# Kernel tuning notes

Hardware: AMD Instinct MI355X
Metric: run time of the kernel (lower is better)

## Reference

```python
import jax, jax.numpy as jnp
import numpy as np

HEAD_COUNT = 16
HEAD_DIM = 128  # embed_count // head_count = 2048 // 16


def setup_inputs() -> dict:
    key = jax.random.key(0)
    k0, k1, k2, k3, k4 = jax.random.split(key, 5)
    B, C, S = 4, 2048, 1024
    keys = jax.random.normal(k0, (B, C, 1, S), dtype=jnp.float32)
    values = jax.random.normal(k1, (B, C, 1, S), dtype=jnp.float32)
    queries = jax.random.normal(k2, (B, C, 1, S), dtype=jnp.float32)
    attention_mask = jax.random.randint(k3, (B, S), 0, 2).astype(bool)
    # guarantee at least one valid key per batch row so softmax is finite
    attention_mask = attention_mask.at[:, 0].set(True)
    w_out = jax.random.normal(k4, (C, C), dtype=jnp.float32) * 0.02
    return {"keys": keys, "values": values, "queries": queries,
            "attention_mask": attention_mask, "w_out": w_out}


def reference(keys, values, queries, attention_mask, w_out):
    B, C, _, S = keys.shape
    h, d = HEAD_COUNT, HEAD_DIM
    # keys: [B,C,1,S] -> transpose(1,3) -> [B,S,1,C] -> [B,S,h,d]
    k = jnp.transpose(keys[:, :, 0, :], (0, 2, 1)).reshape(B, S, h, d)      # bkhd
    # values/queries: [B,C,1,S] -> [B,h,d,S] -> transpose(1,2) -> [B,d,h,S]
    v = jnp.transpose(values[:, :, 0, :].reshape(B, h, d, S), (0, 2, 1, 3))  # bdhk
    q = jnp.transpose(queries[:, :, 0, :].reshape(B, h, d, S), (0, 2, 1, 3)) # bdhq
    # additive mask bias: 0 where attended, -inf where masked; broadcast over h,q
    bias = jnp.where(attention_mask, 0.0, -jnp.inf).astype(keys.dtype)       # [B,K]
    scale = 1.0 / np.sqrt(d).astype(np.float32)
    w = jnp.einsum('bdhq,bkhd->bkhq', q * scale, k)                          # [B,K,h,Q]
    w = w + bias[:, :, None, None]
    w = jax.nn.softmax(w, axis=1)  # softmax over keys (dim 1)
    hid = jnp.einsum('bkhq,bdhk->bdhq', w, v)                                # [B,d,h,Q]
    hid = jnp.transpose(hid, (0, 2, 1, 3)).reshape(B, C, S)                  # [B,C,Q]
    out = jnp.einsum('oc,bcq->boq', w_out, hid)                              # 1x1 conv out_proj
    return out.reshape(B, C, 1, S)
```

## Files before the change

### kernel.cpp

```cpp
#include <hip/hip_runtime.h>

#define Bq 4
#define Cc 2048
#define Ss 1024
#define Hh 16
#define Dd 128

#define QSCALE 0.127517429f

typedef __bf16 bf16x8 __attribute__((ext_vector_type(8)));
typedef float  f32x4  __attribute__((ext_vector_type(4)));

__device__ __forceinline__ ushort f2bf(float f) {
    uint u = __float_as_uint(f);
    u += 0x7FFFu + ((u >> 16) & 1u);
    return (ushort)(u >> 16);
}
__device__ __forceinline__ uint pack2bf(float a, float b) {
    return (uint)f2bf(a) | ((uint)f2bf(b) << 16);
}
__device__ __forceinline__ void gld16(const void* g, void* l) {
    __builtin_amdgcn_global_load_lds(
        (const __attribute__((address_space(1))) unsigned int*)g,
        (__attribute__((address_space(3))) unsigned int*)l, 16, 0, 0);
}

__global__ __launch_bounds__(256) void prep_all3(const float* __restrict__ w,
                                                 const float* __restrict__ v,
                                                 const float* __restrict__ keys,
                                                 const unsigned* __restrict__ mask,
                                                 ushort* __restrict__ wb,
                                                 ushort* __restrict__ vb,
                                                 ushort* __restrict__ Kt,
                                                 float* __restrict__ bias) {
    __shared__ __align__(16) float T[128][65];
    const int t = threadIdx.x;
    const int blk = blockIdx.x;

    if (blk < 2048) {
        const size_t e = ((size_t)blk * 256 + t) * 8;
        const int row = (int)(e >> 11), col = (int)(e & 2047);
        const int colS = (col & ~63) | ((col & 63) ^ ((row & 7) << 3));
        float4 v0 = *(const float4*)&w[e];
        float4 v1 = *(const float4*)&w[e + 4];
        uint4 o;
        o.x = pack2bf(v0.x, v0.y); o.y = pack2bf(v0.z, v0.w);
        o.z = pack2bf(v1.x, v1.y); o.w = pack2bf(v1.z, v1.w);
        *(uint4*)&wb[(size_t)row * 2048 + colS] = o;
    } else if (blk < 6144) {
        const int tid = (blk - 2048) * 256 + t;
        const int row = tid >> 7;
        const int cp = tid & 127;
        const int blk64 = (cp >> 3) * 64;
        const int j0 = cp & 7;
        const int b5 = j0 >> 2, h = j0 & 3;
        const float* src = v + (size_t)row * 1024 + blk64 + 32 * b5 + 4 * h;
        float4 A = *(const float4*)src;
        float4 B = *(const float4*)(src + 16);
        uint4 o;
        o.x = pack2bf(A.x, A.y); o.y = pack2bf(A.z, A.w);
        o.z = pack2bf(B.x, B.y); o.w = pack2bf(B.z, B.w);
        *(uint4*)&vb[(size_t)row * 1024 + blk64 + ((j0 * 8) ^ ((row & 7) << 3))] = o;
    } else if (blk < 7168) {
        const int b2 = blk - 6144;
        const int s0 = (b2 & 15) * 64;
        const int bh = b2 >> 4;
        const float* src = keys + (size_t)bh * 128 * 1024;
#pragma unroll
        for (int p = 0; p < 8; ++p) {
            const int d = p * 16 + (t >> 4);
            float4 v4 = *(const float4*)&src[(size_t)d * 1024 + s0 + (t & 15) * 4];
            T[d][(t & 15) * 4 + 0] = v4.x;
            T[d][(t & 15) * 4 + 1] = v4.y;
            T[d][(t & 15) * 4 + 2] = v4.z;
            T[d][(t & 15) * 4 + 3] = v4.w;
        }
        __syncthreads();
#pragma unroll
        for (int p = 0; p < 4; ++p) {
            const int k = p * 16 + (t >> 4);
            const int x = t & 15;
            uint4 o;
            o.x = pack2bf(T[x * 8 + 0][k], T[x * 8 + 1][k]);
            o.y = pack2bf(T[x * 8 + 2][k], T[x * 8 + 3][k]);
            o.z = pack2bf(T[x * 8 + 4][k], T[x * 8 + 5][k]);
            o.w = pack2bf(T[x * 8 + 6][k], T[x * 8 + 7][k]);
            const size_t rowbyte = ((size_t)bh * 1024 + s0 + k) * 256;
            const int boff = (x * 16) ^ ((k & 7) << 4);
            *(uint4*)((char*)Kt + rowbyte + boff) = o;
        }
    } else {
        __shared__ int f01, ff;
        if (t == 0) { f01 = 0; ff = 0; }
        __syncthreads();
        int a = 0, c = 0;
        for (int i = t; i < 1024; i += 256) {
            unsigned vv = mask[i];
            if (vv != 0u && vv != 1u) a = 1;
            if (vv != 0u && vv != 0x3F800000u) c = 1;
        }
        if (a) atomicOr(&f01, 1);
        if (c) atomicOr(&ff, 1);
        __syncthreads();
        const int mode = f01 ? (ff ? 1 : 2) : 0;
        const int* mi = (const int*)mask;
        const unsigned char* mb = (const unsigned char*)mask;
        const float* mf = (const float*)mask;
        for (int i = t; i < Bq * Ss; i += 256) {
            bool on;
            if (mode == 0)      on = (mi[i] != 0);
            else if (mode == 1) on = (mb[i] != 0);
            else                on = (mf[i] != 0.0f);
            bias[i] = on ? 0.0f : -1e30f;
        }
    }
}

__global__ __launch_bounds__(512) void attn11(const float* __restrict__ queries,
                                              const ushort* __restrict__ Kt,
                                              const ushort* __restrict__ Vbf,
                                              const float* __restrict__ bias,
                                              ushort* __restrict__ hidT) {
    __shared__ __align__(16) char SMEM[102400];
    float* biasS = (float*)(SMEM + 98304);

    const int t = threadIdx.x, l = t & 63, w = t >> 6;
    const int kk = l & 15, g = l >> 4;

    const int bid = blockIdx.x;
    const int vid = (bid & 7) * 32 + (bid >> 3);
    const int bh = vid >> 2, qt = vid & 3;
    const int b = bh >> 4, hh = bh & 15;
    const int q0 = qt * 256;
    const size_t bhbase = (size_t)bh * 1024;

    for (int i = t; i < Ss; i += 512) biasS[i] = bias[b * Ss + i];

    bf16x8 qf[2][4];
    {
        const float* Qg = queries + (size_t)(b * Cc + hh * Dd) * Ss;
        float* Qstg = (float*)SMEM;
#pragma unroll
        for (int half = 0; half < 2; ++half) {
#pragma unroll
            for (int it = 0; it < 8; ++it) {
                const int row = it * 8 + w;
                gld16(Qg + (size_t)(half * 64 + row) * 1024 + q0 + l * 4,
                      (char*)Qstg + row * 1024);
            }
            asm volatile("s_waitcnt vmcnt(0)" ::: "memory");
            __builtin_amdgcn_s_barrier();
#pragma unroll
            for (int dch = 0; dch < 2; ++dch) {
                const int dc = half * 2 + dch;
#pragma unroll
                for (int qs = 0; qs < 2; ++qs) {
                    const int q = w * 32 + qs * 16 + kk;
                    float f[8];
#pragma unroll
                    for (int j = 0; j < 8; ++j) {
                        const int dl = dc * 32 + g * 8 + j - half * 64;
                        f[j] = Qstg[dl * 256 + q];
                    }
                    uint4 u;
                    u.x = pack2bf(f[0] * QSCALE, f[1] * QSCALE);
                    u.y = pack2bf(f[2] * QSCALE, f[3] * QSCALE);
                    u.z = pack2bf(f[4] * QSCALE, f[5] * QSCALE);
                    u.w = pack2bf(f[6] * QSCALE, f[7] * QSCALE);
                    qf[qs][dc] = *(bf16x8*)&u;
                }
            }
            __builtin_amdgcn_s_barrier();
        }
    }

    float lrun[2] = {0.0f, 0.0f};
    f32x4 hacc[2][8];
#pragma unroll
    for (int qs = 0; qs < 2; ++qs)
#pragma unroll
        for (int i = 0; i < 8; ++i) hacc[qs][i] = (f32x4){0.f, 0.f, 0.f, 0.f};

#define ATTN_STAGE(bufi, cki)                                                   \
    {                                                                           \
        const int k0n = (cki) * 64;                                             \
        ushort* Kd = (ushort*)SMEM + (bufi) * 8192;                             \
        ushort* Vd = (ushort*)(SMEM + 49152) + (bufi) * 8192;                   \
        _Pragma("unroll")                                                       \
        for (int ii = 0; ii < 4; ++ii) {                                        \
            const int inst = ii * 8 + w;                                        \
            if (inst < 16) {                                                    \
                gld16(Kt + (bhbase + k0n + inst * 4 + (l >> 4)) * 128 +         \
                          (l & 15) * 8,                                         \
                      Kd + inst * 512);                                         \
            } else {                                                            \
                const int i2 = inst - 16;                                       \
                gld16(Vbf + ((size_t)bh * 128 + i2 * 8 + (l >> 3)) * 1024 +     \
                          k0n + (l & 7) * 8,                                    \
                      Vd + i2 * 512);                                           \
            }                                                                   \
        }                                                                       \
    }

#define QK_HALF(h)                                                               \
    _Pragma("unroll")                                                            \
    for (int n2 = 0; n2 < 2; ++n2) {                                             \
        const int ns = 2 * (h) + n2;                                             \
        const f32x4 ci = *(const f32x4*)&biasS[k0 + ns * 16 + g * 4];            \
        bf16x8 kf[4];                                                            \
        const ushort* kr = KTb + (ns * 16 + kk) * 128;                           \
        _Pragma("unroll")                                                        \
        for (int dc = 0; dc < 4; ++dc)                                           \
            kf[dc] = *(const bf16x8*)(kr + ((dc * 32 + g * 8) ^ ((kk & 7) << 3)));\
        _Pragma("unroll")                                                        \
        for (int qs = 0; qs < 2; ++qs) {                                         \
            f32x4 a = ci;                                                        \
            _Pragma("unroll")                                                    \
            for (int dc = 0; dc < 4; ++dc)                                       \
                a = __builtin_amdgcn_mfma_f32_16x16x32_bf16(                     \
                    kf[dc], qf[qs][dc], a, 0, 0, 0);                             \
            sc[qs][ns] = a;                                                      \
        }                                                                        \
    }

#define SM_HALF(h)                                                               \
    _Pragma("unroll")                                                            \
    for (int qs = 0; qs < 2; ++qs) {                                             \
        float pv0[4], pv1[4];                                                    \
        _Pragma("unroll")                                                        \
        for (int r = 0; r < 4; ++r) {                                            \
            pv0[r] = exp2f(sc[qs][2 * (h)][r]);                                  \
            pv1[r] = exp2f(sc[qs][2 * (h) + 1][r]);                              \
        }                                                                        \
        lrun[qs] += (pv0[0] + pv0[1] + pv0[2] + pv0[3])                          \
                  + (pv1[0] + pv1[1] + pv1[2] + pv1[3]);                         \
        bf16x8 vpk;                                                              \
        _Pragma("unroll")                                                        \
        for (int j = 0; j < 4; ++j) { vpk[j] = (__bf16)pv0[j];                   \
                                      vpk[j + 4] = (__bf16)pv1[j]; }             \
        pb[qs][h] = vpk;                                                         \
    }

#define PV_HALF(h)                                                               \
    _Pragma("unroll")                                                            \
    for (int ds = 0; ds < 8; ++ds) {                                             \
        bf16x8 vf = *(const bf16x8*)(Vsb + (ds * 16 + kk) * 64 +                 \
                        (((h) * 32 + g * 8) ^ ((kk & 7) << 3)));                 \
        hacc[0][ds] = __builtin_amdgcn_mfma_f32_16x16x32_bf16(                   \
            vf, pb[0][h], hacc[0][ds], 0, 0, 0);                                 \
        hacc[1][ds] = __builtin_amdgcn_mfma_f32_16x16x32_bf16(                   \
            vf, pb[1][h], hacc[1][ds], 0, 0, 0);                                 \
    }

#define ATTN_COMPUTE(bi, ck)                                                     \
    {                                                                            \
        const int k0 = (ck) * 64;                                                \
        const ushort* KTb = (const ushort*)SMEM + (bi) * 8192;                   \
        const ushort* Vsb = (const ushort*)(SMEM + 49152) + (bi) * 8192;         \
        f32x4 sc[2][4];                                                          \
        bf16x8 pb[2][2];                                                         \
        QK_HALF(0);                                                              \
        QK_HALF(1);                                                              \
        SM_HALF(0);                                                              \
        PV_HALF(0);                                                              \
        SM_HALF(1);                                                              \
        PV_HALF(1);                                                              \
    }

    ATTN_STAGE(0, 0);
    ATTN_STAGE(1, 1);
    asm volatile("s_waitcnt vmcnt(4)" ::: "memory");
    __builtin_amdgcn_s_barrier();

    int cb = 0, sb = 2;
    for (int ck = 0; ck < 14; ++ck) {
        ATTN_STAGE(sb, ck + 2);
        ATTN_COMPUTE(cb, ck);
        asm volatile("s_waitcnt vmcnt(4)" ::: "memory");
        __builtin_amdgcn_s_barrier();
        cb = (cb == 2) ? 0 : cb + 1;
        sb = (sb == 2) ? 0 : sb + 1;
    }
    ATTN_COMPUTE(cb, 14);
    asm volatile("s_waitcnt vmcnt(0)" ::: "memory");
    __builtin_amdgcn_s_barrier();
    cb = (cb == 2) ? 0 : cb + 1;
    ATTN_COMPUTE(cb, 15);
#undef ATTN_STAGE
#undef ATTN_COMPUTE
#undef QK_HALF
#undef SM_HALF
#undef PV_HALF

    float linv[2];
#pragma unroll
    for (int qs = 0; qs < 2; ++qs) {
        float s = lrun[qs];
        s += __shfl_xor(s, 16);
        s += __shfl_xor(s, 32);
        linv[qs] = 1.0f / s;
    }

    __syncthreads();
    {
        ushort* hs = (ushort*)SMEM;
#pragma unroll
        for (int qs = 0; qs < 2; ++qs) {
            const int row = w * 32 + qs * 16 + kk;
#pragma unroll
            for (int ds = 0; ds < 8; ++ds) {
                uint2 pk;
                pk.x = pack2bf(hacc[qs][ds][0] * linv[qs], hacc[qs][ds][1] * linv[qs]);
                pk.y = pack2bf(hacc[qs][ds][2] * linv[qs], hacc[qs][ds][3] * linv[qs]);
                const int off = row * 256 + ((ds * 32 + g * 8) ^ ((row & 7) << 4));
                *(uint2*)((char*)hs + off) = pk;
            }
        }
    }
    __syncthreads();

    const char* hsb = (const char*)SMEM;
#pragma unroll
    for (int it = 0; it < 8; ++it) {
        const int idx = it * 512 + t;
        const int q = idx >> 4, x = idx & 15;
        uint4 vv = *(const uint4*)(hsb + q * 256 + x * 16);
        *(uint4*)((char*)hidT + ((size_t)(b * Ss + q0 + q)) * 4096 + hh * 256 + x * 16) = vv;
    }
}

__global__ __launch_bounds__(512, 2) void proj5(const ushort* __restrict__ Wbf,
                                                const ushort* __restrict__ hidT,
                                                float* __restrict__ out) {
    __shared__ __align__(16) char SMEM[147456];
    const int t = threadIdx.x, l = t & 63, w = t >> 6;
    const int kk = l & 15, g = l >> 4;
    const int wr = w >> 2, wc = w & 3;

    const int bid = blockIdx.x;
    const int vid = (bid & 7) * 32 + (bid >> 3);
    const int o0 = (vid & 15) * 128;
    const int n0 = (vid >> 4) * 256;

    f32x4 acc[4][4];
#pragma unroll
    for (int i = 0; i < 4; ++i)
#pragma unroll
        for (int j = 0; j < 4; ++j) acc[i][j] = (f32x4){0.f, 0.f, 0.f, 0.f};

    const int swz = (kk & 7) << 3;

#define P5_STAGE_A(st, ks)                                                      \
    {                                                                           \
        ushort* Ad = (ushort*)SMEM + (st) * 8192;                               \
        _Pragma("unroll")                                                       \
        for (int ii = 0; ii < 2; ++ii) {                                        \
            const int idx = ii * 512 + t;                                       \
            gld16(Wbf + (size_t)(o0 + (idx >> 3)) * 2048 + (ks) * 64 +          \
                      (idx & 7) * 8,                                            \
                  Ad + idx * 8);                                                \
        }                                                                       \
    }
#define P5_STAGE_B(st, ks, p)                                                   \
    {                                                                           \
        ushort* Bd = (ushort*)(SMEM + 49152) + (st) * 16384;                    \
        _Pragma("unroll")                                                       \
        for (int jj = (p) * 2; jj < (p) * 2 + 2; ++jj) {                        \
            const int idx = jj * 512 + t;                                       \
            gld16(hidT + (size_t)(n0 + (idx >> 3)) * 2048 + (ks) * 64 +         \
                      (idx & 7) * 8,                                            \
                  Bd + idx * 8);                                                \
        }                                                                       \
    }
#define P5_READ(dcv)                                                            \
    _Pragma("unroll")                                                           \
    for (int ms = 0; ms < 4; ++ms)                                              \
        af[ms] = *(const bf16x8*)&Ab[(wr * 64 + ms * 16 + kk) * 64 +            \
                                     (((dcv) * 32 + g * 8) ^ swz)];             \
    _Pragma("unroll")                                                           \
    for (int ns = 0; ns < 4; ++ns)                                              \
        bfr[ns] = *(const bf16x8*)&Bb[(wc * 64 + ns * 16 + kk) * 64 +           \
                                      (((dcv) * 32 + g * 8) ^ swz)];
#define P5_MFMA()                                                               \
    __builtin_amdgcn_s_setprio(1);                                              \
    _Pragma("unroll")                                                           \
    for (int ms = 0; ms < 4; ++ms)                                              \
        _Pragma("unroll")                                                       \
        for (int ns = 0; ns < 4; ++ns)                                          \
            acc[ms][ns] = __builtin_amdgcn_mfma_f32_16x16x32_bf16(              \
                af[ms], bfr[ns], acc[ms][ns], 0, 0, 0);                         \
    __builtin_amdgcn_s_setprio(0);

    P5_STAGE_A(0, 0); P5_STAGE_B(0, 0, 0); P5_STAGE_B(0, 0, 1);
    P5_STAGE_A(1, 1); P5_STAGE_B(1, 1, 0); P5_STAGE_B(1, 1, 1);
    asm volatile("s_waitcnt vmcnt(6)" ::: "memory");
    __builtin_amdgcn_s_barrier();

    int ct = 0, st2 = 2;
    for (int tt = 0; tt < 32; ++tt) {
        const ushort* Ab = (const ushort*)SMEM + ct * 8192;
        const ushort* Bb = (const ushort*)(SMEM + 49152) + ct * 16384;
        bf16x8 af[4], bfr[4];

        P5_READ(0);
        if (tt < 30) { P5_STAGE_A(st2, tt + 2); P5_STAGE_B(st2, tt + 2, 0); }
        __builtin_amdgcn_s_barrier();
        asm volatile("s_waitcnt lgkmcnt(0)" ::: "memory");
        P5_MFMA();
        __builtin_amdgcn_s_barrier();

        P5_READ(1);
        if (tt < 30) P5_STAGE_B(st2, tt + 2, 1);
        if (tt < 30) { asm volatile("s_waitcnt vmcnt(6)" ::: "memory"); }
        else         { asm volatile("s_waitcnt vmcnt(0)" ::: "memory"); }
        __builtin_amdgcn_s_barrier();
        asm volatile("s_waitcnt lgkmcnt(0)" ::: "memory");
        P5_MFMA();
        __builtin_amdgcn_s_barrier();

        ct = (ct == 2) ? 0 : ct + 1;
        st2 = (st2 == 2) ? 0 : st2 + 1;
    }
#undef P5_STAGE_A
#undef P5_STAGE_B
#undef P5_READ
#undef P5_MFMA

#pragma unroll
    for (int ms = 0; ms < 4; ++ms)
#pragma unroll
        for (int ns = 0; ns < 4; ++ns) {
            const int o = o0 + wr * 64 + ms * 16 + g * 4;
            const int n = n0 + wc * 64 + ns * 16 + kk;
            const int bb = n >> 10, qq = n & 1023;
            float* op = out + ((size_t)(bb * Cc + o)) * Ss + qq;
#pragma unroll
            for (int r = 0; r < 4; ++r) op[(size_t)r * Ss] = acc[ms][ns][r];
        }
}

extern "C" void kernel_launch(void* const* d_in, const int* in_sizes, int n_in,
                              void* d_out, int out_size, void* d_ws, size_t ws_size,
                              hipStream_t stream) {
    const float*    keys    = (const float*)d_in[0];
    const float*    values  = (const float*)d_in[1];
    const float*    queries = (const float*)d_in[2];
    const unsigned* mask    = (const unsigned*)d_in[3];
    const float*    w_out   = (const float*)d_in[4];
    float* out = (float*)d_out;

    char* ws = (char*)d_ws;
    float*  bias = (float*)ws;
    ushort* Wbf  = (ushort*)(ws + 16384);
    ushort* Kt   = (ushort*)(ws + 16384 + (8u << 20));
    ushort* Vbf  = (ushort*)(ws + 16384 + (24u << 20));
    ushort* hidT = (ushort*)(ws + 16384 + (40u << 20));

    hipLaunchKernelGGL(prep_all3, dim3(7169), dim3(256), 0, stream,
                       w_out, values, keys, mask, Wbf, Vbf, Kt, bias);
    hipLaunchKernelGGL(attn11, dim3(256), dim3(512), 0, stream,
                       queries, Kt, Vbf, bias, hidT);
    hipLaunchKernelGGL(proj5, dim3(256), dim3(512), 0, stream,
                       Wbf, hidT, out);
}
```

Measured before the change: 115.8 us.

## Read K/V fragments directly from global memory in attention, drop LDS pipelining

The attention kernel no longer stages K and V tiles through a triple-buffered LDS pipeline. Each wave now loads its MFMA fragments straight from global memory (relying on L1/L2), so the XOR swizzle in the prep kernel is removed. Blocks shrink to 256 threads covering 128 queries, launched as 512 blocks with far less LDS per block, which allows higher occupancy. s_setprio is raised around the MFMA phases. The cost is uncoalesced, latency-bound global fragment loads that have no explicit prefetch or overlap.

Result: slower. 187.3 us (+61.7%).

```diff
diff --git a/kernel.cpp b/kernel.cpp
--- a/kernel.cpp
+++ b/kernel.cpp
@@ -60,7 +60,7 @@
         uint4 o;
         o.x = pack2bf(A.x, A.y); o.y = pack2bf(A.z, A.w);
         o.z = pack2bf(B.x, B.y); o.w = pack2bf(B.z, B.w);
-        *(uint4*)&vb[(size_t)row * 1024 + blk64 + ((j0 * 8) ^ ((row & 7) << 3))] = o;
+        *(uint4*)&vb[(size_t)row * 1024 + blk64 + j0 * 8] = o;
     } else if (blk < 7168) {
         const int b2 = blk - 6144;
         const int s0 = (b2 & 15) * 64;
@@ -86,8 +86,7 @@
             o.z = pack2bf(T[x * 8 + 4][k], T[x * 8 + 5][k]);
             o.w = pack2bf(T[x * 8 + 6][k], T[x * 8 + 7][k]);
             const size_t rowbyte = ((size_t)bh * 1024 + s0 + k) * 256;
-            const int boff = (x * 16) ^ ((k & 7) << 4);
-            *(uint4*)((char*)Kt + rowbyte + boff) = o;
+            *(uint4*)((char*)Kt + rowbyte + x * 16) = o;
         }
     } else {
         __shared__ int f01, ff;
@@ -116,25 +115,24 @@
     }
 }
 
-__global__ __launch_bounds__(512) void attn11(const float* __restrict__ queries,
+__global__ __launch_bounds__(256) void attn12(const float* __restrict__ queries,
                                               const ushort* __restrict__ Kt,
                                               const ushort* __restrict__ Vbf,
                                               const float* __restrict__ bias,
                                               ushort* __restrict__ hidT) {
-    __shared__ __align__(16) char SMEM[102400];
-    float* biasS = (float*)(SMEM + 98304);
+    __shared__ __align__(16) char SMEM[36864];
+    float* biasS = (float*)(SMEM + 32768);
 
     const int t = threadIdx.x, l = t & 63, w = t >> 6;
     const int kk = l & 15, g = l >> 4;
 
     const int bid = blockIdx.x;
-    const int vid = (bid & 7) * 32 + (bid >> 3);
-    const int bh = vid >> 2, qt = vid & 3;
+    const int vid = (bid & 7) * 64 + (bid >> 3);
+    const int bh = vid >> 3, qt = vid & 7;
     const int b = bh >> 4, hh = bh & 15;
-    const int q0 = qt * 256;
-    const size_t bhbase = (size_t)bh * 1024;
-
-    for (int i = t; i < Ss; i += 512) biasS[i] = bias[b * Ss + i];
+    const int q0 = qt * 128;
+
+    for (int i = t; i < Ss; i += 256) biasS[i] = bias[b * Ss + i];
 
     bf16x8 qf[2][4];
     {
@@ -144,12 +142,13 @@
         for (int half = 0; half < 2; ++half) {
 #pragma unroll
             for (int it = 0; it < 8; ++it) {
-                const int row = it * 8 + w;
-                gld16(Qg + (size_t)(half * 64 + row) * 1024 + q0 + l * 4,
-                      (char*)Qstg + row * 1024);
+                const int i2 = it * 4 + w;
+                gld16(Qg + (size_t)(half * 64 + 2 * i2 + (l >> 5)) * 1024 +
+                          q0 + (l & 31) * 4,
+                      (char*)Qstg + i2 * 1024);
             }
             asm volatile("s_waitcnt vmcnt(0)" ::: "memory");
-            __builtin_amdgcn_s_barrier();
+            __syncthreads();
 #pragma unroll
             for (int dch = 0; dch < 2; ++dch) {
                 const int dc = half * 2 + dch;
@@ -159,8 +158,8 @@
                     float f[8];
 #pragma unroll
                     for (int j = 0; j < 8; ++j) {
-                        const int dl = dc * 32 + g * 8 + j - half * 64;
-                        f[j] = Qstg[dl * 256 + q];
+                        const int dl = dch * 32 + g * 8 + j;
+                        f[j] = Qstg[dl * 128 + q];
                     }
                     uint4 u;
                     u.x = pack2bf(f[0] * QSCALE, f[1] * QSCALE);
@@ -170,7 +169,7 @@
                     qf[qs][dc] = *(bf16x8*)&u;
                 }
             }
-            __builtin_amdgcn_s_barrier();
+            __syncthreads();
         }
     }
 
@@ -181,116 +180,74 @@
 #pragma unroll
         for (int i = 0; i < 8; ++i) hacc[qs][i] = (f32x4){0.f, 0.f, 0.f, 0.f};
 
-#define ATTN_STAGE(bufi, cki)                                                   \
-    {                                                                           \
-        const int k0n = (cki) * 64;                                             \
-        ushort* Kd = (ushort*)SMEM + (bufi) * 8192;                             \
-        ushort* Vd = (ushort*)(SMEM + 49152) + (bufi) * 8192;                   \
-        _Pragma("unroll")                                                       \
-        for (int ii = 0; ii < 4; ++ii) {                                        \
-            const int inst = ii * 8 + w;                                        \
-            if (inst < 16) {                                                    \
-                gld16(Kt + (bhbase + k0n + inst * 4 + (l >> 4)) * 128 +         \
-                          (l & 15) * 8,                                         \
-                      Kd + inst * 512);                                         \
-            } else {                                                            \
-                const int i2 = inst - 16;                                       \
-                gld16(Vbf + ((size_t)bh * 128 + i2 * 8 + (l >> 3)) * 1024 +     \
-                          k0n + (l & 7) * 8,                                    \
-                      Vd + i2 * 512);                                           \
-            }                                                                   \
-        }                                                                       \
-    }
-
-#define QK_HALF(h)                                                               \
-    _Pragma("unroll")                                                            \
-    for (int n2 = 0; n2 < 2; ++n2) {                                             \
-        const int ns = 2 * (h) + n2;                                             \
-        const f32x4 ci = *(const f32x4*)&biasS[k0 + ns * 16 + g * 4];            \
-        bf16x8 kf[4];                                                            \
-        const ushort* kr = KTb + (ns * 16 + kk) * 128;                           \
-        _Pragma("unroll")                                                        \
-        for (int dc = 0; dc < 4; ++dc)                                           \
-            kf[dc] = *(const bf16x8*)(kr + ((dc * 32 + g * 8) ^ ((kk & 7) << 3)));\
-        _Pragma("unroll")                                                        \
-        for (int qs = 0; qs < 2; ++qs) {                                         \
-            f32x4 a = ci;                                                        \
-            _Pragma("unroll")                                                    \
-            for (int dc = 0; dc < 4; ++dc)                                       \
-                a = __builtin_amdgcn_mfma_f32_16x16x32_bf16(                     \
-                    kf[dc], qf[qs][dc], a, 0, 0, 0);                             \
-            sc[qs][ns] = a;                                                      \
-        }                                                                        \
-    }
-
-#define SM_HALF(h)                                                               \
-    _Pragma("unroll")                                                            \
-    for (int qs = 0; qs < 2; ++qs) {                                             \
-        float pv0[4], pv1[4];                                                    \
-        _Pragma("unroll")                                                        \
-        for (int r = 0; r < 4; ++r) {                                            \
-            pv0[r] = exp2f(sc[qs][2 * (h)][r]);                                  \
-            pv1[r] = exp2f(sc[qs][2 * (h) + 1][r]);                              \
-        }                                                                        \
-        lrun[qs] += (pv0[0] + pv0[1] + pv0[2] + pv0[3])                          \
-                  + (pv1[0] + pv1[1] + pv1[2] + pv1[3]);                         \
-        bf16x8 vpk;                                                              \
-        _Pragma("unroll")                                                        \
-        for (int j = 0; j < 4; ++j) { vpk[j] = (__bf16)pv0[j];                   \
-                                      vpk[j + 4] = (__bf16)pv1[j]; }             \
-        pb[qs][h] = vpk;                                                         \
-    }
-
-#define PV_HALF(h)                                                               \
-    _Pragma("unroll")                                                            \
-    for (int ds = 0; ds < 8; ++ds) {                                             \
-        bf16x8 vf = *(const bf16x8*)(Vsb + (ds * 16 + kk) * 64 +                 \
-                        (((h) * 32 + g * 8) ^ ((kk & 7) << 3)));                 \
-        hacc[0][ds] = __builtin_amdgcn_mfma_f32_16x16x32_bf16(                   \
-            vf, pb[0][h], hacc[0][ds], 0, 0, 0);                                 \
-        hacc[1][ds] = __builtin_amdgcn_mfma_f32_16x16x32_bf16(                   \
-            vf, pb[1][h], hacc[1][ds], 0, 0, 0);                                 \
-    }
-
-#define ATTN_COMPUTE(bi, ck)                                                     \
-    {                                                                            \
-        const int k0 = (ck) * 64;                                                \
-        const ushort* KTb = (const ushort*)SMEM + (bi) * 8192;                   \
-        const ushort* Vsb = (const ushort*)(SMEM + 49152) + (bi) * 8192;         \
-        f32x4 sc[2][4];                                                          \
-        bf16x8 pb[2][2];                                                         \
-        QK_HALF(0);                                                              \
-        QK_HALF(1);                                                              \
-        SM_HALF(0);                                                              \
-        PV_HALF(0);                                                              \
-        SM_HALF(1);                                                              \
-        PV_HALF(1);                                                              \
-    }
-
-    ATTN_STAGE(0, 0);
-    ATTN_STAGE(1, 1);
-    asm volatile("s_waitcnt vmcnt(4)" ::: "memory");
-    __builtin_amdgcn_s_barrier();
-
-    int cb = 0, sb = 2;
-    for (int ck = 0; ck < 14; ++ck) {
-        ATTN_STAGE(sb, ck + 2);
-        ATTN_COMPUTE(cb, ck);
-        asm volatile("s_waitcnt vmcnt(4)" ::: "memory");
-        __builtin_amdgcn_s_barrier();
-        cb = (cb == 2) ? 0 : cb + 1;
-        sb = (sb == 2) ? 0 : sb + 1;
-    }
-    ATTN_COMPUTE(cb, 14);
-    asm volatile("s_waitcnt vmcnt(0)" ::: "memory");
-    __builtin_amdgcn_s_barrier();
-    cb = (cb == 2) ? 0 : cb + 1;
-    ATTN_COMPUTE(cb, 15);
-#undef ATTN_STAGE
-#undef ATTN_COMPUTE
-#undef QK_HALF
-#undef SM_HALF
-#undef PV_HALF
+    const ushort* Kbh = Kt + (size_t)bh * 1024 * 128;
+    const ushort* Vbh = Vbf + (size_t)bh * 128 * 1024;
+
+#pragma unroll 1
+    for (int ck = 0; ck < 16; ++ck) {
+        const int k0 = ck * 64;
+
+        f32x4 sc[2][4];
+        __builtin_amdgcn_s_setprio(1);
+#pragma unroll
+        for (int ns = 0; ns < 4; ++ns) {
+            const f32x4 ci = *(const f32x4*)&biasS[k0 + ns * 16 + g * 4];
+            const ushort* kr = Kbh + (size_t)(k0 + ns * 16 + kk) * 128;
+            bf16x8 kf[4];
+#pragma unroll
+            for (int dc = 0; dc < 4; ++dc)
+                kf[dc] = *(const bf16x8*)(kr + dc * 32 + g * 8);
+#pragma unroll
+            for (int qs = 0; qs < 2; ++qs) {
+                f32x4 a = ci;
+#pragma unroll
+                for (int dc = 0; dc < 4; ++dc)
+                    a = __builtin_amdgcn_mfma_f32_16x16x32_bf16(
+                        kf[dc], qf[qs][dc], a, 0, 0, 0);
+                sc[qs][ns] = a;
+            }
+        }
+        __builtin_amdgcn_s_setprio(0);
+
+        bf16x8 pb[2][2];
+#pragma unroll
+        for (int qs = 0; qs < 2; ++qs) {
+            float pv[4][4];
+            float s = 0.0f;
+#pragma unroll
+            for (int ns = 0; ns < 4; ++ns)
+#pragma unroll
+                for (int r = 0; r < 4; ++r) {
+                    float p = exp2f(sc[qs][ns][r]);
+                    pv[ns][r] = p;
+                    s += p;
+                }
+            lrun[qs] += s;
+#pragma unroll
+            for (int kh = 0; kh < 2; ++kh) {
+                bf16x8 vpk;
+#pragma unroll
+                for (int j = 0; j < 8; ++j)
+                    vpk[j] = (__bf16)pv[2 * kh + (j >> 2)][j & 3];
+                pb[qs][kh] = vpk;
+            }
+        }
+
+        __builtin_amdgcn_s_setprio(1);
+#pragma unroll
+        for (int kh = 0; kh < 2; ++kh) {
+#pragma unroll
+            for (int ds = 0; ds < 8; ++ds) {
+                bf16x8 vf = *(const bf16x8*)(Vbh + (size_t)(ds * 16 + kk) * 1024 +
+                                             k0 + kh * 32 + g * 8);
+                hacc[0][ds] = __builtin_amdgcn_mfma_f32_16x16x32_bf16(
+                    vf, pb[0][kh], hacc[0][ds], 0, 0, 0);
+                hacc[1][ds] = __builtin_amdgcn_mfma_f32_16x16x32_bf16(
+                    vf, pb[1][kh], hacc[1][ds], 0, 0, 0);
+            }
+        }
+        __builtin_amdgcn_s_setprio(0);
+    }
 
     float linv[2];
 #pragma unroll
@@ -322,7 +279,7 @@
     const char* hsb = (const char*)SMEM;
 #pragma unroll
     for (int it = 0; it < 8; ++it) {
-        const int idx = it * 512 + t;
+        const int idx = it * 256 + t;
         const int q = idx >> 4, x = idx & 15;
         uint4 vv = *(const uint4*)(hsb + q * 256 + x * 16);
         *(uint4*)((char*)hidT + ((size_t)(b * Ss + q0 + q)) * 4096 + hh * 256 + x * 16) = vv;
@@ -458,7 +415,7 @@
 
     hipLaunchKernelGGL(prep_all3, dim3(7169), dim3(256), 0, stream,
                        w_out, values, keys, mask, Wbf, Vbf, Kt, bias);
-    hipLaunchKernelGGL(attn11, dim3(256), dim3(512), 0, stream,
+    hipLaunchKernelGGL(attn12, dim3(512), dim3(256), 0, stream,
                        queries, Kt, Vbf, bias, hidT);
     hipLaunchKernelGGL(proj5, dim3(256), dim3(512), 0, stream,
                        Wbf, hidT, out);
```

## Switch attention MFMAs from 16x16x32 to 32x32x16 bf16 tiles

Applied to the files above, without the earlier changes.

Rewrites the attention kernel's QK and PV inner loops to use 32x32x16 bf16 MFMA instructions instead of 16x16x32. The Q fragment, accumulator and LDS access patterns and the V pre-permutation in the prep kernel are reworked to match the new operand layouts, and the row-sum reduction gets simpler. Instruction priority hints are wrapped around the MFMA loops. The aim is fewer MFMA issues and fewer LDS fragment reads per tile; the cost is more accumulator registers and the need for layout correctness across the two kernels.

Result: no change. 116.2 us (+0.3%).

```diff
diff --git a/kernel.cpp b/kernel.cpp
--- a/kernel.cpp
+++ b/kernel.cpp
@@ -10,6 +10,7 @@
 
 typedef __bf16 bf16x8 __attribute__((ext_vector_type(8)));
 typedef float  f32x4  __attribute__((ext_vector_type(4)));
+typedef float  f32x16 __attribute__((ext_vector_type(16)));
 
 __device__ __forceinline__ ushort f2bf(float f) {
     uint u = __float_as_uint(f);
@@ -53,10 +54,10 @@
         const int cp = tid & 127;
         const int blk64 = (cp >> 3) * 64;
         const int j0 = cp & 7;
-        const int b5 = j0 >> 2, h = j0 & 3;
-        const float* src = v + (size_t)row * 1024 + blk64 + 32 * b5 + 4 * h;
+        const int base = (j0 >> 1) * 16 + (j0 & 1) * 4;
+        const float* src = v + (size_t)row * 1024 + blk64 + base;
         float4 A = *(const float4*)src;
-        float4 B = *(const float4*)(src + 16);
+        float4 B = *(const float4*)(src + 8);
         uint4 o;
         o.x = pack2bf(A.x, A.y); o.y = pack2bf(A.z, A.w);
         o.z = pack2bf(B.x, B.y); o.w = pack2bf(B.z, B.w);
@@ -116,7 +117,7 @@
     }
 }
 
-__global__ __launch_bounds__(512) void attn11(const float* __restrict__ queries,
+__global__ __launch_bounds__(512) void attn13(const float* __restrict__ queries,
                                               const ushort* __restrict__ Kt,
                                               const ushort* __restrict__ Vbf,
                                               const float* __restrict__ bias,
@@ -125,7 +126,8 @@
     float* biasS = (float*)(SMEM + 98304);
 
     const int t = threadIdx.x, l = t & 63, w = t >> 6;
-    const int kk = l & 15, g = l >> 4;
+    const int l31 = l & 31, hi = l >> 5;
+    const int swz = (l31 & 7) << 4;
 
     const int bid = blockIdx.x;
     const int vid = (bid & 7) * 32 + (bid >> 3);
@@ -136,10 +138,11 @@
 
     for (int i = t; i < Ss; i += 512) biasS[i] = bias[b * Ss + i];
 
-    bf16x8 qf[2][4];
+    bf16x8 qf[8];
     {
         const float* Qg = queries + (size_t)(b * Cc + hh * Dd) * Ss;
         float* Qstg = (float*)SMEM;
+        const int q = w * 32 + l31;
 #pragma unroll
         for (int half = 0; half < 2; ++half) {
 #pragma unroll
@@ -148,38 +151,30 @@
                 gld16(Qg + (size_t)(half * 64 + row) * 1024 + q0 + l * 4,
                       (char*)Qstg + row * 1024);
             }
-            asm volatile("s_waitcnt vmcnt(0)" ::: "memory");
-            __builtin_amdgcn_s_barrier();
-#pragma unroll
-            for (int dch = 0; dch < 2; ++dch) {
-                const int dc = half * 2 + dch;
-#pragma unroll
-                for (int qs = 0; qs < 2; ++qs) {
-                    const int q = w * 32 + qs * 16 + kk;
-                    float f[8];
-#pragma unroll
-                    for (int j = 0; j < 8; ++j) {
-                        const int dl = dc * 32 + g * 8 + j - half * 64;
-                        f[j] = Qstg[dl * 256 + q];
-                    }
-                    uint4 u;
-                    u.x = pack2bf(f[0] * QSCALE, f[1] * QSCALE);
-                    u.y = pack2bf(f[2] * QSCALE, f[3] * QSCALE);
-                    u.z = pack2bf(f[4] * QSCALE, f[5] * QSCALE);
-                    u.w = pack2bf(f[6] * QSCALE, f[7] * QSCALE);
-                    qf[qs][dc] = *(bf16x8*)&u;
-                }
+            __syncthreads();
+#pragma unroll
+            for (int dmL = 0; dmL < 4; ++dmL) {
+                float f[8];
+#pragma unroll
+                for (int j = 0; j < 8; ++j)
+                    f[j] = Qstg[(dmL * 16 + hi * 8 + j) * 256 + q];
+                uint4 u;
+                u.x = pack2bf(f[0] * QSCALE, f[1] * QSCALE);
+                u.y = pack2bf(f[2] * QSCALE, f[3] * QSCALE);
+                u.z = pack2bf(f[4] * QSCALE, f[5] * QSCALE);
+                u.w = pack2bf(f[6] * QSCALE, f[7] * QSCALE);
+                qf[half * 4 + dmL] = *(bf16x8*)&u;
             }
-            __builtin_amdgcn_s_barrier();
-        }
-    }
-
-    float lrun[2] = {0.0f, 0.0f};
-    f32x4 hacc[2][8];
-#pragma unroll
-    for (int qs = 0; qs < 2; ++qs)
-#pragma unroll
-        for (int i = 0; i < 8; ++i) hacc[qs][i] = (f32x4){0.f, 0.f, 0.f, 0.f};
+            __syncthreads();
+        }
+    }
+
+    float lrun = 0.0f;
+    f32x16 hacc[4];
+#pragma unroll
+    for (int ds = 0; ds < 4; ++ds)
+#pragma unroll
+        for (int r = 0; r < 16; ++r) hacc[ds][r] = 0.0f;
 
 #define ATTN_STAGE(bufi, cki)                                                   \
     {                                                                           \
@@ -202,69 +197,70 @@
         }                                                                       \
     }
 
-#define QK_HALF(h)                                                               \
-    _Pragma("unroll")                                                            \
-    for (int n2 = 0; n2 < 2; ++n2) {                                             \
-        const int ns = 2 * (h) + n2;                                             \
-        const f32x4 ci = *(const f32x4*)&biasS[k0 + ns * 16 + g * 4];            \
-        bf16x8 kf[4];                                                            \
-        const ushort* kr = KTb + (ns * 16 + kk) * 128;                           \
+#define QK_SUB(ks, scv)                                                          \
+    {                                                                            \
+        f32x16 a;                                                                \
         _Pragma("unroll")                                                        \
-        for (int dc = 0; dc < 4; ++dc)                                           \
-            kf[dc] = *(const bf16x8*)(kr + ((dc * 32 + g * 8) ^ ((kk & 7) << 3)));\
+        for (int qd = 0; qd < 4; ++qd) {                                         \
+            f32x4 cv = *(const f32x4*)&biasS[k0 + (ks) * 32 + qd * 8 + hi * 4];  \
+            a[qd * 4 + 0] = cv[0]; a[qd * 4 + 1] = cv[1];                        \
+            a[qd * 4 + 2] = cv[2]; a[qd * 4 + 3] = cv[3];                        \
+        }                                                                        \
+        const char* kr = KTb + ((ks) * 32 + l31) * 256;                          \
+        __builtin_amdgcn_s_setprio(1);                                           \
         _Pragma("unroll")                                                        \
-        for (int qs = 0; qs < 2; ++qs) {                                         \
-            f32x4 a = ci;                                                        \
+        for (int dm = 0; dm < 8; ++dm) {                                         \
+            bf16x8 kf = *(const bf16x8*)(kr + ((dm * 32 + hi * 16) ^ swz));      \
+            a = __builtin_amdgcn_mfma_f32_32x32x16_bf16(kf, qf[dm], a, 0, 0, 0); \
+        }                                                                        \
+        __builtin_amdgcn_s_setprio(0);                                           \
+        scv = a;                                                                 \
+    }
+
+#define SM_SUB(scv, p0, p1)                                                      \
+    {                                                                            \
+        float s = 0.0f;                                                          \
+        _Pragma("unroll")                                                        \
+        for (int j = 0; j < 8; ++j) {                                            \
+            float e = exp2f(scv[j]);  s += e;  p0[j] = (__bf16)e;                \
+        }                                                                        \
+        _Pragma("unroll")                                                        \
+        for (int j = 0; j < 8; ++j) {                                            \
+            float e = exp2f(scv[8 + j]);  s += e;  p1[j] = (__bf16)e;            \
+        }                                                                        \
+        lrun += s;                                                               \
+    }
+
+#define PV_SUB(ks, p0, p1)                                                       \
+    {                                                                            \
+        __builtin_amdgcn_s_setprio(1);                                           \
+        _Pragma("unroll")                                                        \
+        for (int m = 0; m < 2; ++m) {                                            \
+            const int ko = (ks) * 64 + m * 32 + hi * 16;                         \
             _Pragma("unroll")                                                    \
-            for (int dc = 0; dc < 4; ++dc)                                       \
-                a = __builtin_amdgcn_mfma_f32_16x16x32_bf16(                     \
-                    kf[dc], qf[qs][dc], a, 0, 0, 0);                             \
-            sc[qs][ns] = a;                                                      \
+            for (int dsub = 0; dsub < 4; ++dsub) {                               \
+                const int d = dsub * 32 + l31;                                   \
+                bf16x8 vf = *(const bf16x8*)(Vsb + d * 128 + (ko ^ swz));        \
+                hacc[dsub] = __builtin_amdgcn_mfma_f32_32x32x16_bf16(            \
+                    vf, (m == 0 ? p0 : p1), hacc[dsub], 0, 0, 0);                \
+            }                                                                    \
         }                                                                        \
-    }
-
-#define SM_HALF(h)                                                               \
-    _Pragma("unroll")                                                            \
-    for (int qs = 0; qs < 2; ++qs) {                                             \
-        float pv0[4], pv1[4];                                                    \
-        _Pragma("unroll")                                                        \
-        for (int r = 0; r < 4; ++r) {                                            \
-            pv0[r] = exp2f(sc[qs][2 * (h)][r]);                                  \
-            pv1[r] = exp2f(sc[qs][2 * (h) + 1][r]);                              \
-        }                                                                        \
-        lrun[qs] += (pv0[0] + pv0[1] + pv0[2] + pv0[3])                          \
-                  + (pv1[0] + pv1[1] + pv1[2] + pv1[3]);                         \
-        bf16x8 vpk;                                                              \
-        _Pragma("unroll")                                                        \
-        for (int j = 0; j < 4; ++j) { vpk[j] = (__bf16)pv0[j];                   \
-                                      vpk[j + 4] = (__bf16)pv1[j]; }             \
-        pb[qs][h] = vpk;                                                         \
-    }
-
-#define PV_HALF(h)                                                               \
-    _Pragma("unroll")                                                            \
-    for (int ds = 0; ds < 8; ++ds) {                                             \
-        bf16x8 vf = *(const bf16x8*)(Vsb + (ds * 16 + kk) * 64 +                 \
-                        (((h) * 32 + g * 8) ^ ((kk & 7) << 3)));                 \
-        hacc[0][ds] = __builtin_amdgcn_mfma_f32_16x16x32_bf16(                   \
-            vf, pb[0][h], hacc[0][ds], 0, 0, 0);                                 \
-        hacc[1][ds] = __builtin_amdgcn_mfma_f32_16x16x32_bf16(                   \
-            vf, pb[1][h], hacc[1][ds], 0, 0, 0);                                 \
+        __builtin_amdgcn_s_setprio(0);                                           \
     }
 
 #define ATTN_COMPUTE(bi, ck)                                                     \
     {                                                                            \
         const int k0 = (ck) * 64;                                                \
-        const ushort* KTb = (const ushort*)SMEM + (bi) * 8192;                   \
-        const ushort* Vsb = (const ushort*)(SMEM + 49152) + (bi) * 8192;         \
-        f32x4 sc[2][4];                                                          \
-        bf16x8 pb[2][2];                                                         \
-        QK_HALF(0);                                                              \
-        QK_HALF(1);                                                              \
-        SM_HALF(0);                                                              \
-        PV_HALF(0);                                                              \
-        SM_HALF(1);                                                              \
-        PV_HALF(1);                                                              \
+        const char* KTb = SMEM + (bi) * 16384;                                   \
+        const char* Vsb = SMEM + 49152 + (bi) * 16384;                           \
+        f32x16 sc0, sc1;                                                         \
+        bf16x8 p00, p01, p10, p11;                                               \
+        QK_SUB(0, sc0);                                                          \
+        QK_SUB(1, sc1);                                                          \
+        SM_SUB(sc0, p00, p01);                                                   \
+        PV_SUB(0, p00, p01);                                                     \
+        SM_SUB(sc1, p10, p11);                                                   \
+        PV_SUB(1, p10, p11);                                                     \
     }
 
     ATTN_STAGE(0, 0);
@@ -288,34 +284,29 @@
     ATTN_COMPUTE(cb, 15);
 #undef ATTN_STAGE
 #undef ATTN_COMPUTE
-#undef QK_HALF
-#undef SM_HALF
-#undef PV_HALF
-
-    float linv[2];
-#pragma unroll
-    for (int qs = 0; qs < 2; ++qs) {
-        float s = lrun[qs];
-        s += __shfl_xor(s, 16);
-        s += __shfl_xor(s, 32);
-        linv[qs] = 1.0f / s;
-    }
+#undef QK_SUB
+#undef SM_SUB
+#undef PV_SUB
+
+    const float linv = 1.0f / (lrun + __shfl_xor(lrun, 32));
 
     __syncthreads();
     {
         ushort* hs = (ushort*)SMEM;
-#pragma unroll
-        for (int qs = 0; qs < 2; ++qs) {
-            const int row = w * 32 + qs * 16 + kk;
-#pragma unroll
-            for (int ds = 0; ds < 8; ++ds) {
+        const int row = w * 32 + l31;
+        const int rsw = (row & 7) << 4;
+#pragma unroll
+        for (int dsub = 0; dsub < 4; ++dsub)
+#pragma unroll
+            for (int qd = 0; qd < 4; ++qd) {
                 uint2 pk;
-                pk.x = pack2bf(hacc[qs][ds][0] * linv[qs], hacc[qs][ds][1] * linv[qs]);
-                pk.y = pack2bf(hacc[qs][ds][2] * linv[qs], hacc[qs][ds][3] * linv[qs]);
-                const int off = row * 256 + ((ds * 32 + g * 8) ^ ((row & 7) << 4));
+                pk.x = pack2bf(hacc[dsub][qd * 4 + 0] * linv,
+                               hacc[dsub][qd * 4 + 1] * linv);
+                pk.y = pack2bf(hacc[dsub][qd * 4 + 2] * linv,
+                               hacc[dsub][qd * 4 + 3] * linv);
+                const int off = row * 256 + ((dsub * 64 + qd * 16 + hi * 8) ^ rsw);
                 *(uint2*)((char*)hs + off) = pk;
             }
-        }
     }
     __syncthreads();
 
@@ -458,7 +449,7 @@
 
     hipLaunchKernelGGL(prep_all3, dim3(7169), dim3(256), 0, stream,
                        w_out, values, keys, mask, Wbf, Vbf, Kt, bias);
-    hipLaunchKernelGGL(attn11, dim3(256), dim3(512), 0, stream,
+    hipLaunchKernelGGL(attn13, dim3(256), dim3(512), 0, stream,
                        queries, Kt, Vbf, bias, hidT);
     hipLaunchKernelGGL(proj5, dim3(256), dim3(512), 0, stream,
                        Wbf, hidT, out);
```
